# Kernel tuning notes

Hardware: AMD Instinct MI355X
Metric: run time of the kernel (lower is better)

## Reference

```python
import jax, jax.numpy as jnp
from jax import lax
import numpy as np

B, L, A = 4096, 168, 128   # batch, attn_length, attn_size
FN, FS = 32, 1             # filter_num, filter_size
FD = A - FS + 1            # feature_dim


def setup_inputs() -> dict:
    key = jax.random.key(0)
    ks = jax.random.split(key, 5)
    return {
        "query": jax.random.normal(ks[0], (B, 2 * A), jnp.float32),
        "attn_states": jax.random.normal(ks[1], (B, L, A), jnp.float32),
        "W_q": jax.random.normal(ks[2], (2 * A, FN), jnp.float32) / np.sqrt(2 * A),
        "conv_k": jax.random.normal(ks[3], (L, FS, 1, FN), jnp.float32) / np.sqrt(L * FS),
        "conv_b": jnp.zeros((FN,), jnp.float32),
        "W_out": jax.random.normal(ks[4], (2 * A + FN, A), jnp.float32) / np.sqrt(2 * A + FN),
        "b_out": jnp.zeros((A,), jnp.float32),
    }


def reference(query, attn_states, W_q, conv_k, conv_b, W_out, b_out):
    # w: [B, FN] -- Dense(filter_num, no bias)(query)
    w = query @ W_q
    # Conv2D over [B, L, A, 1] with kernel [L, FS] 'VALID' -> [B, 1, FD, FN]
    x = attn_states[..., None]
    cv = lax.conv_general_dilated(
        x, conv_k, window_strides=(1, 1), padding='VALID',
        dimension_numbers=('NHWC', 'HWIO', 'NHWC')) + conv_b
    cv = cv[:, 0]                                   # [B, FD, FN]
    # sigmoid-gated attention score over filter dim
    s = jnp.einsum('bfk,bk->bf', cv, w)             # [B, FD]
    a = jax.nn.sigmoid(s)
    d = jnp.einsum('bf,bfk->bk', a, cv)             # [B, FN]
    new_attns = jnp.concatenate([query, d], axis=1) @ W_out + b_out  # [B, A]
    new_attn_states = attn_states[:, 1:, :]         # [B, L-1, A]
    return new_attns, new_attn_states
```

## Files before the change

kernel.cpp:

```cpp
#include <hip/hip_runtime.h>
#include <math.h>

#define BB  4096
#define LL  168
#define AA  128
#define FNN 32

typedef float f16v __attribute__((ext_vector_type(16)));

__global__ __launch_bounds__(256, 4)
void tpa_fused(const float* __restrict__ query,
               const float* __restrict__ attn_states,
               const float* __restrict__ W_q,
               const float* __restrict__ conv_k,
               const float* __restrict__ conv_b,
               const float* __restrict__ W_out,
               const float* __restrict__ b_out,
               float* __restrict__ out_attns,
               float* __restrict__ out_states)
{
    const int b    = blockIdx.x;
    const int t    = threadIdx.x;
    const int lane = t & 63;
    const int wid  = __builtin_amdgcn_readfirstlane(t >> 6);
    const int h    = wid & 1;
    const int p    = wid >> 1;

    __shared__ float qrow[256];
    __shared__ float red[512];
    __shared__ float sh_wv[32];
    __shared__ float sh_a[128];
    __shared__ float sh_dp[64];
    __shared__ float sh_d[32];

    qrow[t] = query[(size_t)b * 256 + t];
    __syncthreads();

    {
        const int n = t & 31, kc = t >> 5;
        float pp = 0.f;
        #pragma unroll
        for (int i = 0; i < 32; ++i) {
            const int k = (kc << 5) + i;
            pp += qrow[k] * W_q[k * FNN + n];
        }
        red[t] = pp;
    }
    __syncthreads();
    if (t < 32) {
        float s = 0.f;
        #pragma unroll
        for (int kc = 0; kc < 8; ++kc) s += red[(kc << 5) + t];
        sh_wv[t] = s;
    }
    __syncthreads();

    float wvv[16];
    #pragma unroll
    for (int n = 0; n < 16; ++n) wvv[n] = sh_wv[h * 16 + n];

    float cv0[16], cv1[16];
    #pragma unroll
    for (int n = 0; n < 16; ++n) { cv0[n] = 0.f; cv1[n] = 0.f; }

    const float* asp = attn_states + (size_t)b * (LL * AA) + p * AA + lane * 2;
    float*       osp = out_states  + (size_t)b * ((LL - 1) * AA) + lane * 2;
    const float* kwp = conv_k + h * 16;
    const bool dostore = (h == 0);

    float2 a_cur = *(const float2*)asp;
    f16v   k_cur = *(const f16v*)(kwp + p * FNN);
    float2 a_nxt;
    f16v   k_nxt;

    for (int i = 0; i < 84; i += 2) {
        a_nxt = *(const float2*)(asp + (size_t)(i + 1) * 256);
        k_nxt = *(const f16v*)(kwp + (size_t)(2 * (i + 1) + p) * FNN);
        if (dostore) {
            const int ro = 2 * i + p - 1;
            if (ro >= 0) *(float2*)(osp + (size_t)ro * AA) = a_cur;
        }
        #pragma unroll
        for (int n = 0; n < 16; ++n) {
            cv0[n] += a_cur.x * k_cur[n];
            cv1[n] += a_cur.y * k_cur[n];
        }
        if (i + 2 < 84) {
            a_cur = *(const float2*)(asp + (size_t)(i + 2) * 256);
            k_cur = *(const f16v*)(kwp + (size_t)(2 * (i + 2) + p) * FNN);
        }
        if (dostore) {
            const int ro = 2 * i + 1 + p;
            *(float2*)(osp + (size_t)ro * AA) = a_nxt;
        }
        #pragma unroll
        for (int n = 0; n < 16; ++n) {
            cv0[n] += a_nxt.x * k_nxt[n];
            cv1[n] += a_nxt.y * k_nxt[n];
        }
    }

    if (p == 0) {
        #pragma unroll
        for (int n = 0; n < 16; ++n) {
            const float cb = conv_b[h * 16 + n];
            cv0[n] += cb;
            cv1[n] += cb;
        }
    }

    float sp0 = 0.f, sp1 = 0.f;
    #pragma unroll
    for (int n = 0; n < 16; ++n) { sp0 += cv0[n] * wvv[n]; sp1 += cv1[n] * wvv[n]; }
    red[(lane * 2 + 0) * 4 + wid] = sp0;
    red[(lane * 2 + 1) * 4 + wid] = sp1;
    __syncthreads();
    if (t < 128) {
        const float s = red[t * 4] + red[t * 4 + 1] + red[t * 4 + 2] + red[t * 4 + 3];
        sh_a[t] = 1.f / (1.f + expf(-s));
    }
    __syncthreads();

    const float a0 = sh_a[lane * 2], a1 = sh_a[lane * 2 + 1];
    float dp[16];
    #pragma unroll
    for (int n = 0; n < 16; ++n) dp[n] = a0 * cv0[n] + a1 * cv1[n];
    #pragma unroll
    for (int off = 32; off > 0; off >>= 1) {
        #pragma unroll
        for (int n = 0; n < 16; ++n) dp[n] += __shfl_xor(dp[n], off);
    }
    if (lane == 0) {
        #pragma unroll
        for (int n = 0; n < 16; ++n) sh_dp[wid * 16 + n] = dp[n];
    }
    __syncthreads();
    if (t < 32) sh_d[t] = sh_dp[t] + sh_dp[t + 32];
    __syncthreads();

    {
        const int m = t & 127, khalf = t >> 7;
        float acc = 0.f;
        const int kbase = khalf << 7;
        #pragma unroll 4
        for (int k = kbase; k < kbase + 128; ++k)
            acc += qrow[k] * W_out[k * AA + m];
        if (khalf) {
            #pragma unroll
            for (int j = 0; j < 32; ++j)
                acc += sh_d[j] * W_out[(256 + j) * AA + m];
        } else {
            acc += b_out[m];
        }
        red[t] = acc;
    }
    __syncthreads();
    if (t < 128)
        out_attns[(size_t)b * AA + t] = red[t] + red[t + 128];
}

extern "C" void kernel_launch(void* const* d_in, const int* in_sizes, int n_in,
                              void* d_out, int out_size, void* d_ws, size_t ws_size,
                              hipStream_t stream) {
    const float* query       = (const float*)d_in[0];
    const float* attn_states = (const float*)d_in[1];
    const float* W_q         = (const float*)d_in[2];
    const float* conv_k      = (const float*)d_in[3];
    const float* conv_b      = (const float*)d_in[4];
    const float* W_out       = (const float*)d_in[5];
    const float* b_out       = (const float*)d_in[6];

    float* out_attns  = (float*)d_out;
    float* out_states = (float*)d_out + (size_t)BB * AA;

    tpa_fused<<<BB, 256, 0, stream>>>(query, attn_states, W_q, conv_k, conv_b,
                                      W_out, b_out, out_attns, out_states);
}
```

Before: 690.1 us.

## Stage conv kernel in LDS, deepen attn_states prefetch, split state copy across halves

Copies the whole conv kernel (168x32 floats) into shared memory per block, so the inner loop reads weights from LDS as float4 instead of scalar/vector global loads. The attn_states stream now uses a six-deep register prefetch ring, and the out_states copy is shared between the two h-waves by alternating rows. Launch bounds move to 6 blocks per SM to raise occupancy. The cost is about 21KB of extra LDS per block, which may limit occupancy, plus a per-block global-to-LDS copy of the kernel weights.

New measurement: 2.066 ms. +199.3%, slower.

```diff
diff --git a/kernel.cpp b/kernel.cpp
--- a/kernel.cpp
+++ b/kernel.cpp
@@ -6,9 +6,7 @@
 #define AA  128
 #define FNN 32
 
-typedef float f16v __attribute__((ext_vector_type(16)));
-
-__global__ __launch_bounds__(256, 4)
+__global__ __launch_bounds__(256, 6)
 void tpa_fused(const float* __restrict__ query,
                const float* __restrict__ attn_states,
                const float* __restrict__ W_q,
@@ -26,6 +24,7 @@
     const int h    = wid & 1;
     const int p    = wid >> 1;
 
+    __shared__ float sh_k[LL * FNN];
     __shared__ float qrow[256];
     __shared__ float red[512];
     __shared__ float sh_wv[32];
@@ -34,6 +33,9 @@
     __shared__ float sh_d[32];
 
     qrow[t] = query[(size_t)b * 256 + t];
+    #pragma unroll
+    for (int j = 0; j < 21; ++j)
+        sh_k[j * 256 + t] = conv_k[j * 256 + t];
     __syncthreads();
 
     {
@@ -55,48 +57,47 @@
     }
     __syncthreads();
 
-    float wvv[16];
-    #pragma unroll
-    for (int n = 0; n < 16; ++n) wvv[n] = sh_wv[h * 16 + n];
-
     float cv0[16], cv1[16];
     #pragma unroll
     for (int n = 0; n < 16; ++n) { cv0[n] = 0.f; cv1[n] = 0.f; }
 
-    const float* asp = attn_states + (size_t)b * (LL * AA) + p * AA + lane * 2;
-    float*       osp = out_states  + (size_t)b * ((LL - 1) * AA) + lane * 2;
-    const float* kwp = conv_k + h * 16;
-    const bool dostore = (h == 0);
+    const float* asp   = attn_states + (size_t)b * (LL * AA) + p * AA + lane * 2;
+    float*       osp   = out_states  + (size_t)b * ((LL - 1) * AA) + lane * 2;
+    const float* kbase = sh_k + h * 16;
 
-    float2 a_cur = *(const float2*)asp;
-    f16v   k_cur = *(const f16v*)(kwp + p * FNN);
-    float2 a_nxt;
-    f16v   k_nxt;
+    float2 ab[6];
+    #pragma unroll
+    for (int j = 0; j < 6; ++j)
+        ab[j] = *(const float2*)(asp + (size_t)j * 256);
 
-    for (int i = 0; i < 84; i += 2) {
-        a_nxt = *(const float2*)(asp + (size_t)(i + 1) * 256);
-        k_nxt = *(const f16v*)(kwp + (size_t)(2 * (i + 1) + p) * FNN);
-        if (dostore) {
-            const int ro = 2 * i + p - 1;
-            if (ro >= 0) *(float2*)(osp + (size_t)ro * AA) = a_cur;
-        }
+    for (int i = 0; i < 84; i += 6) {
         #pragma unroll
-        for (int n = 0; n < 16; ++n) {
-            cv0[n] += a_cur.x * k_cur[n];
-            cv1[n] += a_cur.y * k_cur[n];
-        }
-        if (i + 2 < 84) {
-            a_cur = *(const float2*)(asp + (size_t)(i + 2) * 256);
-            k_cur = *(const f16v*)(kwp + (size_t)(2 * (i + 2) + p) * FNN);
-        }
-        if (dostore) {
-            const int ro = 2 * i + 1 + p;
-            *(float2*)(osp + (size_t)ro * AA) = a_nxt;
-        }
-        #pragma unroll
-        for (int n = 0; n < 16; ++n) {
-            cv0[n] += a_nxt.x * k_nxt[n];
-            cv1[n] += a_nxt.y * k_nxt[n];
+        for (int j = 0; j < 6; ++j) {
+            const int r = i + j;
+            const float2 av = ab[j];
+
+            int rp = r + 6; if (rp > 83) rp = 83;
+            ab[j] = *(const float2*)(asp + (size_t)rp * 256);
+
+            if ((j & 1) == h) {
+                const int ro = 2 * r + p - 1;
+                if (ro >= 0)
+                    *(float2*)(osp + (size_t)ro * AA) = av;
+            }
+
+            const float* kp = kbase + (2 * r + p) * FNN;
+            #pragma unroll
+            for (int c = 0; c < 4; ++c) {
+                const float4 kv = *(const float4*)(kp + c * 4);
+                cv0[c * 4 + 0] += av.x * kv.x;
+                cv0[c * 4 + 1] += av.x * kv.y;
+                cv0[c * 4 + 2] += av.x * kv.z;
+                cv0[c * 4 + 3] += av.x * kv.w;
+                cv1[c * 4 + 0] += av.y * kv.x;
+                cv1[c * 4 + 1] += av.y * kv.y;
+                cv1[c * 4 + 2] += av.y * kv.z;
+                cv1[c * 4 + 3] += av.y * kv.w;
+            }
         }
     }
 
@@ -111,7 +112,11 @@
 
     float sp0 = 0.f, sp1 = 0.f;
     #pragma unroll
-    for (int n = 0; n < 16; ++n) { sp0 += cv0[n] * wvv[n]; sp1 += cv1[n] * wvv[n]; }
+    for (int n = 0; n < 16; ++n) {
+        const float wvn = sh_wv[h * 16 + n];
+        sp0 += cv0[n] * wvn;
+        sp1 += cv1[n] * wvn;
+    }
     red[(lane * 2 + 0) * 4 + wid] = sp0;
     red[(lane * 2 + 1) * 4 + wid] = sp1;
     __syncthreads();
@@ -141,9 +146,9 @@
     {
         const int m = t & 127, khalf = t >> 7;
         float acc = 0.f;
-        const int kbase = khalf << 7;
+        const int kbase2 = khalf << 7;
         #pragma unroll 4
-        for (int k = kbase; k < kbase + 128; ++k)
+        for (int k = kbase2; k < kbase2 + 128; ++k)
             acc += qrow[k] * W_out[k * AA + m];
         if (khalf) {
             #pragma unroll
```
